# Performance work log

Hardware: AMD Instinct MI355X
Metric: run time of the kernel (lower is better)

The kernel has to match this reference:

```python
import jax, jax.numpy as jnp
import numpy as np

B, P, K_NB, D, H = 4, 1024, 32, 768, 12
S = P + 1
HD = D // H  # 64

def _ln(x, w, b):
    m = jnp.mean(x, -1, keepdims=True)
    v = jnp.var(x, -1, keepdims=True)
    return (x - m) / jnp.sqrt(v + 1e-5) * w + b

def setup_inputs() -> dict:
    key = jax.random.key(0)
    ks = jax.random.split(key, 8)
    w = lambda k, sh: jax.random.normal(k, sh, jnp.float32) * 0.02
    return {
        'x': jax.random.normal(ks[0], (B, S, D), jnp.float32),
        'routes': jax.random.randint(ks[1], (P, K_NB), 0, P, dtype=jnp.int32),
        'qkv_w': w(ks[2], (D, 3 * D)), 'qkv_b': jnp.zeros((3 * D,), jnp.float32),
        'proj_w': w(ks[3], (D, D)), 'proj_b': jnp.zeros((D,), jnp.float32),
        'ln1_w': jnp.ones((D,), jnp.float32), 'ln1_b': jnp.zeros((D,), jnp.float32),
        'ln2_w': jnp.ones((D,), jnp.float32), 'ln2_b': jnp.zeros((D,), jnp.float32),
        'mlp_w1': w(ks[4], (D, 4 * D)), 'mlp_b1': jnp.zeros((4 * D,), jnp.float32),
        'mlp_w2': w(ks[5], (4 * D, D)), 'mlp_b2': jnp.zeros((D,), jnp.float32),
    }

def reference(x, routes, qkv_w, qkv_b, proj_w, proj_b, ln1_w, ln1_b,
              ln2_w, ln2_b, mlp_w1, mlp_b1, mlp_w2, mlp_b2):
    scale = HD ** -0.5
    xn = _ln(x, ln1_w, ln1_b)
    qkv = (xn @ qkv_w + qkv_b).reshape(B, S, 3, H, HD).transpose(2, 0, 3, 1, 4)
    Q, Kt, V = qkv[0], qkv[1], qkv[2]  # each [B,H,S,HD]
    # CLS token: full dense attention over all S tokens
    sc = jnp.einsum('bhqd,bhkd->bhqk', Q[:, :, :1], Kt) * scale
    oc = jnp.einsum('bhqk,bhkd->bhqd', jax.nn.softmax(sc, -1), V)  # [B,H,1,HD]
    # patch tokens: sparse attention over k routed neighbors
    r = routes + 1  # shift past CLS (buffer routes_shifted)
    Kg = Kt[:, :, r, :]  # [B,H,P,k,HD] gathered keys
    Vg = V[:, :, r, :]   # [B,H,P,k,HD] gathered values
    sp = jnp.einsum('bhpd,bhpkd->bhpk', Q[:, :, 1:], Kg) * scale
    op = jnp.einsum('bhpk,bhpkd->bhpd', jax.nn.softmax(sp, -1), Vg)
    out = jnp.concatenate([oc, op], axis=2).transpose(0, 2, 1, 3).reshape(B, S, D)
    x = x + (out @ proj_w + proj_b)
    h = _ln(x, ln2_w, ln2_b)
    h = jax.nn.gelu(h @ mlp_w1 + mlp_b1, approximate=False) @ mlp_w2 + mlp_b2
    return x + h
```

## Files before the change

### kernel.cpp

```cpp
#include <hip/hip_runtime.h>
#include <hip/hip_bf16.h>

using bf16 = __hip_bfloat16;
using s8v  = __attribute__((ext_vector_type(8))) short;
using f4v  = __attribute__((ext_vector_type(4))) float;

constexpr int B_   = 4;
constexpr int P_   = 1024;
constexpr int KNB  = 32;
constexpr int D_   = 768;
constexpr int H_   = 12;
constexpr int S_   = P_ + 1;
constexpr int M_   = B_ * S_;
constexpr int MPAD = 4224;

#define DEVI static __device__ __forceinline__

DEVI float b2f_lo(unsigned u) { return __builtin_bit_cast(float, u << 16); }
DEVI float b2f_hi(unsigned u) { return __builtin_bit_cast(float, u & 0xffff0000u); }
DEVI unsigned short f2bu(float f) {
  return __builtin_bit_cast(unsigned short, __float2bfloat16(f));
}

template<int KK, int NN>
__global__ __launch_bounds__(256)
void wt_conv(const float* __restrict__ W, bf16* __restrict__ Wt) {
  __shared__ float t[32][33];
  int bk = blockIdx.x * 32, bn = blockIdx.y * 32;
  int tx = threadIdx.x & 31, ty = threadIdx.x >> 5;
#pragma unroll
  for (int i = 0; i < 32; i += 8)
    t[ty + i][tx] = W[(size_t)(bk + ty + i) * NN + bn + tx];
  __syncthreads();
#pragma unroll
  for (int i = 0; i < 32; i += 8)
    Wt[(size_t)(bn + ty + i) * KK + bk + tx] = __float2bfloat16(t[tx][ty + i]);
}

__global__ __launch_bounds__(256)
void ln_kernel(const float* __restrict__ x, const float* __restrict__ w,
               const float* __restrict__ b, bf16* __restrict__ out) {
  int row = blockIdx.x;
  const float* xr = x + (size_t)row * D_;
  int t = threadIdx.x;
  float v0 = xr[t], v1 = xr[t + 256], v2 = xr[t + 512];
  float s = v0 + v1 + v2;
  float ss = v0 * v0 + v1 * v1 + v2 * v2;
#pragma unroll
  for (int o = 32; o; o >>= 1) { s += __shfl_xor(s, o); ss += __shfl_xor(ss, o); }
  __shared__ float sm[4], sv[4];
  if ((t & 63) == 0) { sm[t >> 6] = s; sv[t >> 6] = ss; }
  __syncthreads();
  float S = sm[0] + sm[1] + sm[2] + sm[3];
  float SS = sv[0] + sv[1] + sv[2] + sv[3];
  float mean = S * (1.f / D_);
  float var  = SS * (1.f / D_) - mean * mean;
  float inv  = rsqrtf(var + 1e-5f);
  bf16* orow = out + (size_t)row * D_;
  orow[t]       = __float2bfloat16((v0 - mean) * inv * w[t]       + b[t]);
  orow[t + 256] = __float2bfloat16((v1 - mean) * inv * w[t + 256] + b[t + 256]);
  orow[t + 512] = __float2bfloat16((v2 - mean) * inv * w[t + 512] + b[t + 512]);
}

template<int BM, int N, int K, int MODE>
__global__ __launch_bounds__(256)
void gemm_bf16(const bf16* __restrict__ A, const bf16* __restrict__ Bt,
               const float* __restrict__ bias, const float* __restrict__ resid,
               void* __restrict__ dst) {
  constexpr int MR = BM / 32;
  __shared__ bf16 ldsA[2][BM * 32];
  __shared__ bf16 ldsB[2][128 * 32];
  const int tm = blockIdx.x, tn = blockIdx.y;
  const int tid = threadIdx.x;
  const int wid = tid >> 6, lane = tid & 63;
  const int wr = wid >> 1, wc = wid & 1;

  auto stage = [&](int bufi, int step) {
    const int k0 = step * 32;
#pragma unroll
    for (int i = 0; i < BM / 64; ++i) {
      int c = wid * 64 + i * 256 + lane;
      int r = c >> 2, slot = c & 3;
      int gs = slot ^ ((r >> 1) & 3);
      const bf16* ga = A + (size_t)(tm * BM + r) * K + k0 + gs * 8;
      bf16* la = &ldsA[bufi][(wid * 64 + i * 256) * 8];
      __builtin_amdgcn_global_load_lds(
          (__attribute__((address_space(1))) void*)ga,
          (__attribute__((address_space(3))) void*)la, 16, 0, 0);
    }
#pragma unroll
    for (int i = 0; i < 2; ++i) {
      int c = wid * 64 + i * 256 + lane;
      int r = c >> 2, slot = c & 3;
      int gs = slot ^ ((r >> 1) & 3);
      const bf16* ga = Bt + (size_t)(tn * 128 + r) * K + k0 + gs * 8;
      bf16* la = &ldsB[bufi][(wid * 64 + i * 256) * 8];
      __builtin_amdgcn_global_load_lds(
          (__attribute__((address_space(1))) void*)ga,
          (__attribute__((address_space(3))) void*)la, 16, 0, 0);
    }
  };

  f4v acc[MR][4] = {};

  stage(0, 0);
  __syncthreads();
  int buf = 0;
  const int nk = K / 32;
  for (int kt = 0; kt < nk; ++kt) {
    if (kt + 1 < nk) stage(buf ^ 1, kt + 1);
    s8v af[MR], bfv[4];
#pragma unroll
    for (int m = 0; m < MR; ++m) {
      int row = wr * (MR * 16) + m * 16 + (lane & 15);
      int slot = (lane >> 4) ^ ((row >> 1) & 3);
      af[m] = *(const s8v*)&ldsA[buf][row * 32 + slot * 8];
    }
#pragma unroll
    for (int n = 0; n < 4; ++n) {
      int row = wc * 64 + n * 16 + (lane & 15);
      int slot = (lane >> 4) ^ ((row >> 1) & 3);
      bfv[n] = *(const s8v*)&ldsB[buf][row * 32 + slot * 8];
    }
#pragma unroll
    for (int m = 0; m < MR; ++m)
#pragma unroll
      for (int n = 0; n < 4; ++n)
        acc[m][n] = __builtin_amdgcn_mfma_f32_16x16x32_bf16(af[m], bfv[n], acc[m][n], 0, 0, 0);
    __syncthreads();
    buf ^= 1;
  }

#pragma unroll
  for (int m = 0; m < MR; ++m)
#pragma unroll
    for (int n = 0; n < 4; ++n)
#pragma unroll
      for (int j = 0; j < 4; ++j) {
        int row = tm * BM + wr * (MR * 16) + m * 16 + (lane >> 4) * 4 + j;
        int col = tn * 128 + wc * 64 + n * 16 + (lane & 15);
        float v = acc[m][n][j];
        if (MODE == 0) {
          if (row < M_) {
            float val = v + bias[col];
            int which = col / 768, rem = col % 768;
            int bb = row / S_, s = row % S_;
            ((bf16*)dst)[((size_t)(which * B_ + bb) * S_ + s) * 768 + rem] =
                __float2bfloat16(val);
          }
        } else if (MODE == 1) {
          if (row < M_) {
            float val = v + bias[col] + resid[(size_t)row * N + col];
            ((float*)dst)[(size_t)row * N + col] = val;
          }
        } else {
          float val = v + bias[col];
          val = 0.5f * val * (1.f + erff(val * 0.70710678f));
          ((bf16*)dst)[(size_t)row * N + col] = __float2bfloat16(val);
        }
      }
}

__global__ __launch_bounds__(256)
void cls_partial(const bf16* __restrict__ QKV, float* __restrict__ part) {
  int bh = blockIdx.x, c = blockIdx.y;
  int b = bh / H_, h = bh % H_;
  const bf16* q  = QKV + ((size_t)(0 * B_ + b) * S_) * D_ + h * 64;
  const bf16* Kr = QKV + ((size_t)(1 * B_ + b) * S_) * D_ + h * 64;
  const bf16* Vr = QKV + ((size_t)(2 * B_ + b) * S_) * D_ + h * 64;
  int k0 = c * 256, kn = (c == 3) ? 257 : 256;
  __shared__ float qf[64];
  __shared__ float sc[257];
  __shared__ float red[4];
  __shared__ float pv[4][64];
  int t = threadIdx.x;
  if (t < 64) qf[t] = __bfloat162float(q[t]);
  __syncthreads();
  for (int kk = t; kk < kn; kk += 256) {
    const uint4* k4 = (const uint4*)(Kr + (size_t)(k0 + kk) * D_);
    float s = 0.f;
#pragma unroll
    for (int i = 0; i < 8; ++i) {
      uint4 kv = k4[i];
      const float* q8 = &qf[i * 8];
      s += b2f_lo(kv.x) * q8[0] + b2f_hi(kv.x) * q8[1]
         + b2f_lo(kv.y) * q8[2] + b2f_hi(kv.y) * q8[3]
         + b2f_lo(kv.z) * q8[4] + b2f_hi(kv.z) * q8[5]
         + b2f_lo(kv.w) * q8[6] + b2f_hi(kv.w) * q8[7];
    }
    sc[kk] = s * 0.125f;
  }
  __syncthreads();
  float mx = -1e30f;
  for (int kk = t; kk < kn; kk += 256) mx = fmaxf(mx, sc[kk]);
#pragma unroll
  for (int o = 32; o; o >>= 1) mx = fmaxf(mx, __shfl_xor(mx, o));
  if ((t & 63) == 0) red[t >> 6] = mx;
  __syncthreads();
  float M = fmaxf(fmaxf(red[0], red[1]), fmaxf(red[2], red[3]));
  __syncthreads();
  float sum = 0.f;
  for (int kk = t; kk < kn; kk += 256) { float e = __expf(sc[kk] - M); sc[kk] = e; sum += e; }
#pragma unroll
  for (int o = 32; o; o >>= 1) sum += __shfl_xor(sum, o);
  if ((t & 63) == 0) red[t >> 6] = sum;
  __syncthreads();
  float L = red[0] + red[1] + red[2] + red[3];
  int d = t & 63, kg = t >> 6;
  float acc = 0.f;
  for (int kk = kg; kk < kn; kk += 4)
    acc += sc[kk] * __bfloat162float(Vr[(size_t)(k0 + kk) * D_ + d]);
  pv[kg][d] = acc;
  __syncthreads();
  float* pp = part + ((size_t)bh * 4 + c) * 68;
  if (t < 64) pp[4 + t] = pv[0][t] + pv[1][t] + pv[2][t] + pv[3][t];
  else if (t == 64) pp[0] = M;
  else if (t == 65) pp[1] = L;
}

__global__ __launch_bounds__(64)
void cls_combine(const float* __restrict__ part, bf16* __restrict__ out) {
  int bh = blockIdx.x, t = threadIdx.x;
  const float* pp = part + (size_t)bh * 4 * 68;
  float m0 = pp[0], m1 = pp[68], m2 = pp[136], m3 = pp[204];
  float M = fmaxf(fmaxf(m0, m1), fmaxf(m2, m3));
  float e0 = __expf(m0 - M), e1 = __expf(m1 - M), e2 = __expf(m2 - M), e3 = __expf(m3 - M);
  float L = pp[1] * e0 + pp[69] * e1 + pp[137] * e2 + pp[205] * e3;
  float o = pp[4 + t] * e0 + pp[72 + t] * e1 + pp[140 + t] * e2 + pp[208 + t] * e3;
  int b = bh / H_, h = bh % H_;
  out[(size_t)(b * S_) * D_ + h * 64 + t] = __float2bfloat16(o / L);
}

__global__ __launch_bounds__(256)
void routed_attn(const bf16* __restrict__ QKV, const int* __restrict__ routes,
                 bf16* __restrict__ out) {
  int unit = blockIdx.x * 4 + (threadIdx.x >> 6);
  int lane = threadIdx.x & 63;
  int h = unit % H_;
  int bp = unit / H_;
  int p = bp % P_, b = bp / P_;

  int k = lane & 31, hi = lane >> 5;
  int r = routes[p * KNB + k] + 1;

  const bf16* Qp = QKV + ((size_t)(0 * B_ + b) * S_ + (p + 1)) * D_ + h * 64 + hi * 32;
  const bf16* Kb = QKV + ((size_t)(1 * B_ + b) * S_) * D_;
  const bf16* Vb = QKV + ((size_t)(2 * B_ + b) * S_) * D_;

  const uint4* q4 = (const uint4*)Qp;
  const uint4* k4 = (const uint4*)(Kb + (size_t)r * D_ + h * 64 + hi * 32);
  float dot = 0.f;
#pragma unroll
  for (int i = 0; i < 4; ++i) {
    uint4 qv = q4[i], kv = k4[i];
    dot += b2f_lo(kv.x) * b2f_lo(qv.x) + b2f_hi(kv.x) * b2f_hi(qv.x)
         + b2f_lo(kv.y) * b2f_lo(qv.y) + b2f_hi(kv.y) * b2f_hi(qv.y)
         + b2f_lo(kv.z) * b2f_lo(qv.z) + b2f_hi(kv.z) * b2f_hi(qv.z)
         + b2f_lo(kv.w) * b2f_lo(qv.w) + b2f_hi(kv.w) * b2f_hi(qv.w);
  }
  dot += __shfl_xor(dot, 32);
  float sc = dot * 0.125f;

  float mx = sc;
#pragma unroll
  for (int o = 16; o; o >>= 1) mx = fmaxf(mx, __shfl_xor(mx, o));
  float w = __expf(sc - mx);
  float sum = w;
#pragma unroll
  for (int o = 16; o; o >>= 1) sum += __shfl_xor(sum, o);
  float inv = 1.f / sum;

  int c = lane & 7, kr0 = lane >> 3;
  float acc[8] = {};
#pragma unroll
  for (int j = 0; j < 4; ++j) {
    int kj = (kr0 & 7) + 8 * j;
    float wj = __shfl(w, kj);
    int rj = __shfl(r, kj);
    uint4 vv = *(const uint4*)(Vb + (size_t)rj * D_ + h * 64 + c * 8);
    acc[0] += wj * b2f_lo(vv.x); acc[1] += wj * b2f_hi(vv.x);
    acc[2] += wj * b2f_lo(vv.y); acc[3] += wj * b2f_hi(vv.y);
    acc[4] += wj * b2f_lo(vv.z); acc[5] += wj * b2f_hi(vv.z);
    acc[6] += wj * b2f_lo(vv.w); acc[7] += wj * b2f_hi(vv.w);
  }
#pragma unroll
  for (int s = 8; s < 64; s <<= 1)
#pragma unroll
    for (int d = 0; d < 8; ++d) acc[d] += __shfl_xor(acc[d], s);

  if (lane < 8) {
    s8v o;
#pragma unroll
    for (int d = 0; d < 8; ++d) o[d] = (short)f2bu(acc[d] * inv);
    *(s8v*)(out + ((size_t)(b * S_ + p + 1)) * D_ + h * 64 + c * 8) = o;
  }
}

extern "C" void kernel_launch(void* const* d_in, const int* in_sizes, int n_in,
                              void* d_out, int out_size, void* d_ws, size_t ws_size,
                              hipStream_t stream) {
  const float* x      = (const float*)d_in[0];
  const int*   routes = (const int*)d_in[1];
  const float* qkv_w  = (const float*)d_in[2];
  const float* qkv_b  = (const float*)d_in[3];
  const float* proj_w = (const float*)d_in[4];
  const float* proj_b = (const float*)d_in[5];
  const float* ln1_w  = (const float*)d_in[6];
  const float* ln1_b  = (const float*)d_in[7];
  const float* ln2_w  = (const float*)d_in[8];
  const float* ln2_b  = (const float*)d_in[9];
  const float* mlp_w1 = (const float*)d_in[10];
  const float* mlp_b1 = (const float*)d_in[11];
  const float* mlp_w2 = (const float*)d_in[12];
  const float* mlp_b2 = (const float*)d_in[13];
  float* out = (float*)d_out;

  bf16* qkvw_t  = (bf16*)d_ws;
  bf16* projw_t = qkvw_t + 2304 * 768;
  bf16* mlpw1_t = projw_t + 768 * 768;
  bf16* mlpw2_t = mlpw1_t + 3072 * 768;
  bf16* xnA     = mlpw2_t + 768 * 3072;
  bf16* qkvbuf  = xnA + (size_t)MPAD * 768;
  bf16* attn    = qkvbuf + (size_t)3 * B_ * S_ * 768;
  bf16* h2      = attn + (size_t)MPAD * 768;
  bf16* g       = xnA;
  float* clsp   = (float*)(attn + (size_t)M_ * 768);

  wt_conv<768, 2304><<<dim3(24, 72), 256, 0, stream>>>(qkv_w, qkvw_t);
  wt_conv<768, 768><<<dim3(24, 24), 256, 0, stream>>>(proj_w, projw_t);
  wt_conv<768, 3072><<<dim3(24, 96), 256, 0, stream>>>(mlp_w1, mlpw1_t);
  wt_conv<3072, 768><<<dim3(96, 24), 256, 0, stream>>>(mlp_w2, mlpw2_t);

  ln_kernel<<<M_, 256, 0, stream>>>(x, ln1_w, ln1_b, xnA);

  gemm_bf16<128, 2304, 768, 0><<<dim3(33, 18), 256, 0, stream>>>(xnA, qkvw_t, qkv_b, nullptr, qkvbuf);

  routed_attn<<<(B_ * P_ * H_) / 4, 256, 0, stream>>>(qkvbuf, routes, attn);
  cls_partial<<<dim3(B_ * H_, 4), 256, 0, stream>>>(qkvbuf, clsp);
  cls_combine<<<B_ * H_, 64, 0, stream>>>(clsp, attn);

  gemm_bf16<64, 768, 768, 1><<<dim3(66, 6), 256, 0, stream>>>(attn, projw_t, proj_b, x, out);

  ln_kernel<<<M_, 256, 0, stream>>>(out, ln2_w, ln2_b, h2);

  gemm_bf16<128, 3072, 768, 2><<<dim3(33, 24), 256, 0, stream>>>(h2, mlpw1_t, mlp_b1, nullptr, g);

  gemm_bf16<64, 768, 3072, 1><<<dim3(66, 6), 256, 0, stream>>>(g, mlpw2_t, mlp_b2, out, out);
}
```

Measured before the change: 377.8 us.

## Deepen GEMM pipeline to four LDS stages and remap blocks per XCD

The GEMM kernel moves from a double-buffered LDS pipeline with two __syncthreads per k-step to a 4-buffer ring holding three loads in flight. Each step waits with explicit vmcnt counts and a single barrier instead of a full sync. Block indices are launched as a 1D grid and remapped so that consecutive tiles sharing A rows land on the same XCD, which should improve L2 reuse. The costs are more LDS per block, which may lower occupancy, and hand-tuned vmcnt values that must match the number of loads issued per stage.

```diff
diff --git a/kernel.cpp b/kernel.cpp
--- a/kernel.cpp
+++ b/kernel.cpp
@@ -15,6 +15,8 @@
 constexpr int MPAD = 4224;
 
 #define DEVI static __device__ __forceinline__
+#define WAITVM(N) asm volatile("s_waitcnt vmcnt(" #N ")" ::: "memory")
+#define MEMFENCE  asm volatile("" ::: "memory")
 
 DEVI float b2f_lo(unsigned u) { return __builtin_bit_cast(float, u << 16); }
 DEVI float b2f_hi(unsigned u) { return __builtin_bit_cast(float, u & 0xffff0000u); }
@@ -67,10 +69,19 @@
 void gemm_bf16(const bf16* __restrict__ A, const bf16* __restrict__ Bt,
                const float* __restrict__ bias, const float* __restrict__ resid,
                void* __restrict__ dst) {
-  constexpr int MR = BM / 32;
-  __shared__ bf16 ldsA[2][BM * 32];
-  __shared__ bf16 ldsB[2][128 * 32];
-  const int tm = blockIdx.x, tn = blockIdx.y;
+  constexpr int MR   = BM / 32;
+  constexpr int LPS  = BM / 64 + 2;
+  constexpr int TN   = N / 128;
+  constexpr int NBLK = (MPAD / BM) * TN;
+  __shared__ bf16 ldsA[4][BM * 32];
+  __shared__ bf16 ldsB[4][128 * 32];
+
+  int bid = blockIdx.x;
+  constexpr int NQ = NBLK >> 3, NR = NBLK & 7;
+  int xcd = bid & 7, off = bid >> 3;
+  int swz = (xcd < NR ? xcd * (NQ + 1) : NR * (NQ + 1) + (xcd - NR) * NQ) + off;
+  const int tm = swz / TN, tn = swz % TN;
+
   const int tid = threadIdx.x;
   const int wid = tid >> 6, lane = tid & 63;
   const int wr = wid >> 1, wc = wid & 1;
@@ -102,33 +113,43 @@
   };
 
   f4v acc[MR][4] = {};
-
-  stage(0, 0);
-  __syncthreads();
-  int buf = 0;
   const int nk = K / 32;
+
+  stage(0, 0); stage(1, 1); stage(2, 2);
+
+#pragma unroll 4
   for (int kt = 0; kt < nk; ++kt) {
-    if (kt + 1 < nk) stage(buf ^ 1, kt + 1);
+    const int rem = nk - kt;
+    if (rem > 2) {
+      if constexpr (LPS == 4) WAITVM(8); else WAITVM(6);
+    } else if (rem == 2) {
+      if constexpr (LPS == 4) WAITVM(4); else WAITVM(3);
+    } else {
+      WAITVM(0);
+    }
+    __builtin_amdgcn_s_barrier();
+    MEMFENCE;
+    if (kt + 3 < nk) stage((kt + 3) & 3, kt + 3);
+
+    const int cur = kt & 3;
     s8v af[MR], bfv[4];
 #pragma unroll
     for (int m = 0; m < MR; ++m) {
       int row = wr * (MR * 16) + m * 16 + (lane & 15);
       int slot = (lane >> 4) ^ ((row >> 1) & 3);
-      af[m] = *(const s8v*)&ldsA[buf][row * 32 + slot * 8];
+      af[m] = *(const s8v*)&ldsA[cur][row * 32 + slot * 8];
     }
 #pragma unroll
     for (int n = 0; n < 4; ++n) {
       int row = wc * 64 + n * 16 + (lane & 15);
       int slot = (lane >> 4) ^ ((row >> 1) & 3);
-      bfv[n] = *(const s8v*)&ldsB[buf][row * 32 + slot * 8];
+      bfv[n] = *(const s8v*)&ldsB[cur][row * 32 + slot * 8];
     }
 #pragma unroll
     for (int m = 0; m < MR; ++m)
 #pragma unroll
       for (int n = 0; n < 4; ++n)
         acc[m][n] = __builtin_amdgcn_mfma_f32_16x16x32_bf16(af[m], bfv[n], acc[m][n], 0, 0, 0);
-    __syncthreads();
-    buf ^= 1;
   }
 
 #pragma unroll
@@ -143,9 +164,9 @@
         if (MODE == 0) {
           if (row < M_) {
             float val = v + bias[col];
-            int which = col / 768, rem = col % 768;
+            int which = col / 768, rem2 = col % 768;
             int bb = row / S_, s = row % S_;
-            ((bf16*)dst)[((size_t)(which * B_ + bb) * S_ + s) * 768 + rem] =
+            ((bf16*)dst)[((size_t)(which * B_ + bb) * S_ + s) * 768 + rem2] =
                 __float2bfloat16(val);
           }
         } else if (MODE == 1) {
@@ -333,17 +354,17 @@
 
   ln_kernel<<<M_, 256, 0, stream>>>(x, ln1_w, ln1_b, xnA);
 
-  gemm_bf16<128, 2304, 768, 0><<<dim3(33, 18), 256, 0, stream>>>(xnA, qkvw_t, qkv_b, nullptr, qkvbuf);
+  gemm_bf16<128, 2304, 768, 0><<<33 * 18, 256, 0, stream>>>(xnA, qkvw_t, qkv_b, nullptr, qkvbuf);
 
   routed_attn<<<(B_ * P_ * H_) / 4, 256, 0, stream>>>(qkvbuf, routes, attn);
   cls_partial<<<dim3(B_ * H_, 4), 256, 0, stream>>>(qkvbuf, clsp);
   cls_combine<<<B_ * H_, 64, 0, stream>>>(clsp, attn);
 
-  gemm_bf16<64, 768, 768, 1><<<dim3(66, 6), 256, 0, stream>>>(attn, projw_t, proj_b, x, out);
+  gemm_bf16<64, 768, 768, 1><<<66 * 6, 256, 0, stream>>>(attn, projw_t, proj_b, x, out);
 
   ln_kernel<<<M_, 256, 0, stream>>>(out, ln2_w, ln2_b, h2);
 
-  gemm_bf16<128, 3072, 768, 2><<<dim3(33, 24), 256, 0, stream>>>(h2, mlpw1_t, mlp_b1, nullptr, g);
-
-  gemm_bf16<64, 768, 3072, 1><<<dim3(66, 6), 256, 0, stream>>>(g, mlpw2_t, mlp_b2, out, out);
-}
+  gemm_bf16<128, 3072, 768, 2><<<33 * 24, 256, 0, stream>>>(h2, mlpw1_t, mlp_b1, nullptr, g);
+
+  gemm_bf16<64, 768, 3072, 1><<<66 * 6, 256, 0, stream>>>(g, mlpw2_t, mlp_b2, out, out);
+}
```

Measured after the change: 361.7 us. -4.3%, faster.
